# Performance work log

Hardware: AMD Instinct MI355X
Metric: run time of the kernel (lower is better)

Reference implementation:

```python
import jax, jax.numpy as jnp
import numpy as np

V, E, H = 32000, 256, 512
B, S, T = 32, 80, 80


def setup_inputs() -> dict:
    key = jax.random.key(0)
    ks = jax.random.split(key, 16)
    s = 0.05
    emb = jax.random.normal(ks[0], (V, E), jnp.float32) * s
    emb = emb.at[0].set(0.0)  # padding_idx=0 row is zero
    inp = {
        "src": jax.random.randint(ks[1], (B, S), 0, V),
        "tgt": jax.random.randint(ks[2], (B, T), 0, V),
        "emb": emb,
        "enc_Wih": jax.random.normal(ks[3], (3 * H, E), jnp.float32) * s,
        "enc_Whh": jax.random.normal(ks[4], (3 * H, H), jnp.float32) * s,
        "enc_bih": jax.random.normal(ks[5], (3 * H,), jnp.float32) * s,
        "enc_bhh": jax.random.normal(ks[6], (3 * H,), jnp.float32) * s,
        "dec_Wih": jax.random.normal(ks[7], (3 * H, E), jnp.float32) * s,
        "dec_Whh": jax.random.normal(ks[8], (3 * H, H), jnp.float32) * s,
        "dec_bih": jax.random.normal(ks[9], (3 * H,), jnp.float32) * s,
        "dec_bhh": jax.random.normal(ks[10], (3 * H,), jnp.float32) * s,
        "out_W": jax.random.normal(ks[11], (V, 2 * H), jnp.float32) * s,
        "out_b": jax.random.normal(ks[12], (V,), jnp.float32) * s,
    }
    return inp


def _gru_cell(x, h, Wih, Whh, bih, bhh):
    # PyTorch GRU cell: gates ordered (r, z, n)
    gi = x @ Wih.T + bih          # (B, 3H)
    gh = h @ Whh.T + bhh          # (B, 3H)
    i_r, i_z, i_n = jnp.split(gi, 3, axis=-1)
    h_r, h_z, h_n = jnp.split(gh, 3, axis=-1)
    r = jax.nn.sigmoid(i_r + h_r)
    z = jax.nn.sigmoid(i_z + h_z)
    n = jnp.tanh(i_n + r * h_n)
    return (1.0 - z) * n + z * h


def reference(src, tgt, emb, enc_Wih, enc_Whh, enc_bih, enc_bhh,
              dec_Wih, dec_Whh, dec_bih, dec_bhh, out_W, out_b):
    Bsz, Tlen = tgt.shape

    # ---- encoder: single-layer GRU over src ----
    x_src = emb[src]                              # (B, S, E)
    h0 = jnp.zeros((Bsz, H), x_src.dtype)

    def enc_step(h, x_t):
        h = _gru_cell(x_t, h, enc_Wih, enc_Whh, enc_bih, enc_bhh)
        return h, h

    h_enc, enc_outs = jax.lax.scan(enc_step, h0, jnp.swapaxes(x_src, 0, 1))
    enc_outs = jnp.swapaxes(enc_outs, 0, 1)       # (B, S, H)

    # ---- decoder: teacher forcing (ratio=1.0), steps t=1..T-1 ----
    x_dec = emb[tgt[:, :-1]]                      # (B, T-1, E)

    def dec_step(h, x_t):
        h = _gru_cell(x_t, h, dec_Wih, dec_Whh, dec_bih, dec_bhh)
        # Luong dot attention on new hidden state
        scores = jnp.einsum('bsh,bh->bs', enc_outs, h)
        aw = jax.nn.softmax(scores, axis=1)
        ctx = jnp.einsum('bs,bsh->bh', aw, enc_outs)
        combined = jnp.concatenate([h, ctx], axis=1)   # (B, 2H)
        step_logits = combined @ out_W.T + out_b       # (B, V)
        return h, step_logits

    _, step_logits = jax.lax.scan(dec_step, h_enc, jnp.swapaxes(x_dec, 0, 1))
    step_logits = jnp.swapaxes(step_logits, 0, 1)      # (B, T-1, V)

    # logits[:, 0, :] stays zero, matching the torch module
    logits = jnp.concatenate(
        [jnp.zeros((Bsz, 1, V), step_logits.dtype), step_logits], axis=1)
    return logits
```

## Files before the change

kernel.cpp:

```cpp
#include <hip/hip_runtime.h>

#define VV 32000
#define EE 256
#define HH 512
#define BB 32
#define SS 80
#define TT 80

typedef __attribute__((ext_vector_type(8))) _Float16 half8;
typedef __attribute__((ext_vector_type(4))) _Float16 half4;
typedef __attribute__((ext_vector_type(4))) float floatx4;
typedef unsigned long long u64;

__device__ __forceinline__ void gload16(const _Float16* g, _Float16* l) {
  __builtin_amdgcn_global_load_lds((const __attribute__((address_space(1))) void*)g,
                                   (__attribute__((address_space(3))) void*)l, 16, 0, 0);
}

__device__ __forceinline__ u64 aload(const u64* p) {
  return __hip_atomic_load(p, __ATOMIC_RELAXED, __HIP_MEMORY_SCOPE_AGENT);
}
__device__ __forceinline__ void astore(u64* p, u64 v) {
  __hip_atomic_store(p, v, __ATOMIC_RELAXED, __HIP_MEMORY_SCOPE_AGENT);
}

__device__ __forceinline__ unsigned pack15(unsigned short u) {
  return (u & 0x3FFFu) | ((u >> 1) & 0x4000u);
}
__device__ __forceinline__ unsigned short unpack15(unsigned v) {
  return (unsigned short)((v & 0x3FFFu) | ((v & 0x4000u) << 1));
}
__device__ __forceinline__ u64 unpack_word4(u64 a) {
  u64 o = 0;
#pragma unroll
  for (int i = 0; i < 4; ++i)
    o |= (u64)unpack15((unsigned)(a >> (15*i)) & 0x7FFFu) << (16*i);
  return o;
}

__device__ __forceinline__ float dot8(half8 a, half8 b, float c) {
  typedef __attribute__((ext_vector_type(2))) _Float16 half2v;
  half2v a0 = {a[0],a[1]}, a1 = {a[2],a[3]}, a2 = {a[4],a[5]}, a3 = {a[6],a[7]};
  half2v b0 = {b[0],b[1]}, b1 = {b[2],b[3]}, b2 = {b[4],b[5]}, b3 = {b[6],b[7]};
  c = __builtin_amdgcn_fdot2(a0, b0, c, false);
  c = __builtin_amdgcn_fdot2(a1, b1, c, false);
  c = __builtin_amdgcn_fdot2(a2, b2, c, false);
  c = __builtin_amdgcn_fdot2(a3, b3, c, false);
  return c;
}

__device__ __forceinline__ float sigm(float x) { return 1.f/(1.f + __expf(-x)); }
__device__ __forceinline__ float tanh_f(float x) { return 2.f/(1.f + __expf(-2.f*x)) - 1.f; }

__global__ __launch_bounds__(256) void gi_fused(
    const int* __restrict__ src, const int* __restrict__ tgt,
    const float* __restrict__ emb,
    const float* __restrict__ eWih, const float* __restrict__ ebih,
    const float* __restrict__ dWih, const float* __restrict__ dbih,
    float* __restrict__ giE, float* __restrict__ giD)
{
  __shared__ _Float16 As[4096];
  __shared__ _Float16 Bs[4096];
  const int tid = threadIdx.x;
  const int lane = tid & 63;
  const int wv = tid >> 6;
  const int wr = wv >> 1, wc = wv & 1;
  const int mt = blockIdx.y;
  const bool isE = blockIdx.x < 12;
  const int nt = isE ? blockIdx.x : blockIdx.x - 12;
  const float* Wih = isE ? eWih : dWih;
  const float* bih = isE ? ebih : dbih;
  float* gi = isE ? giE : giD;
  floatx4 acc[4][4];
#pragma unroll
  for (int i=0;i<4;++i)
#pragma unroll
    for (int j=0;j<4;++j) acc[i][j] = (floatx4){0.f,0.f,0.f,0.f};
  const int r2 = tid >> 1, cb = (tid & 1) * 16;
  const int R = mt*128 + r2;
  int tok = -1;
  if (isE) tok = src[R];
  else if (R < 2528) { const int b_ = R/79, tt = R - b_*79; tok = tgt[b_*80 + tt]; }
  const float* arow = (tok >= 0) ? emb + (size_t)tok*EE : nullptr;
  const float* brow = Wih + (size_t)(nt*128 + r2)*EE;
  const int g8 = (lane >> 4) * 8;
  const int lr = lane & 15;
  for (int kb = 0; kb < EE; kb += 32) {
    __syncthreads();
    if (arow) {
#pragma unroll
      for (int q = 0; q < 4; ++q) {
        const floatx4 va = *(const floatx4*)(arow + kb + cb + q*4);
#pragma unroll
        for (int e = 0; e < 4; ++e) As[r2*32 + cb + q*4 + e] = (_Float16)va[e];
      }
    } else {
#pragma unroll
      for (int q = 0; q < 16; ++q) As[r2*32 + cb + q] = (_Float16)0.f;
    }
#pragma unroll
    for (int q = 0; q < 4; ++q) {
      const floatx4 vb = *(const floatx4*)(brow + kb + cb + q*4);
#pragma unroll
      for (int e = 0; e < 4; ++e) Bs[r2*32 + cb + q*4 + e] = (_Float16)vb[e];
    }
    __syncthreads();
    half8 af[4], bf[4];
#pragma unroll
    for (int i=0;i<4;++i) af[i] = *(const half8*)(As + (wr*64 + i*16 + lr)*32 + g8);
#pragma unroll
    for (int j=0;j<4;++j) bf[j] = *(const half8*)(Bs + (wc*64 + j*16 + lr)*32 + g8);
#pragma unroll
    for (int i=0;i<4;++i)
#pragma unroll
      for (int j=0;j<4;++j)
        acc[i][j] = __builtin_amdgcn_mfma_f32_16x16x32_f16(af[i], bf[j], acc[i][j], 0,0,0);
  }
  const int rm = 4*(lane>>4);
#pragma unroll
  for (int i=0;i<4;++i)
#pragma unroll
    for (int r=0;r<4;++r) {
      const int row = mt*128 + wr*64 + i*16 + rm + r;
      if (isE || row < 2528) {
#pragma unroll
        for (int j=0;j<4;++j) {
          const int col = nt*128 + wc*64 + j*16 + lr;
          gi[(size_t)row*1536 + col] = acc[i][j][r] + bih[col];
        }
      }
    }
}

__global__ __launch_bounds__(256) void logits_gemm(
    const _Float16* __restrict__ A,
    const float* __restrict__ Bw,
    const float* __restrict__ bias, float* __restrict__ out)
{
  const int p = blockIdx.x;
  const int x = p & 7, s = p >> 3;
  const int nt = x + 8*(s / 20);
  const int mt = s % 20;
  if (nt >= 250) return;
  __shared__ _Float16 As[4096];
  __shared__ _Float16 Bs[4096];
  const int tid = threadIdx.x;
  const int lane = tid & 63;
  const int wv = tid >> 6;
  const int wr = wv >> 1, wc = wv & 1;
  floatx4 acc[4][4];
#pragma unroll
  for (int i=0;i<4;++i)
#pragma unroll
    for (int j=0;j<4;++j) acc[i][j] = (floatx4){0.f,0.f,0.f,0.f};
  const int srow = lane >> 2;
  const int scol = (lane & 3) * 8;
  const _Float16* Ab = A + (size_t)(mt*128)*1024;
  const int r2 = tid >> 1, cb = (tid & 1) * 16;
  const float* brow = Bw + (size_t)(nt*128 + r2)*1024;
  const int g8 = (lane >> 4) * 8;
  const int lr = lane & 15;
  for (int kb = 0; kb < 1024; kb += 32) {
    __syncthreads();
#pragma unroll
    for (int cc = 0; cc < 2; ++cc) {
      const int c = wv*2 + cc;
      gload16(Ab + (size_t)(c*16 + srow)*1024 + kb + scol, As + c*512);
    }
#pragma unroll
    for (int q = 0; q < 4; ++q) {
      const floatx4 vb = *(const floatx4*)(brow + kb + cb + q*4);
#pragma unroll
      for (int e = 0; e < 4; ++e) Bs[r2*32 + cb + q*4 + e] = (_Float16)vb[e];
    }
    __syncthreads();
    half8 af[4], bf[4];
#pragma unroll
    for (int i=0;i<4;++i) af[i] = *(const half8*)(As + (wr*64 + i*16 + lr)*32 + g8);
#pragma unroll
    for (int j=0;j<4;++j) bf[j] = *(const half8*)(Bs + (wc*64 + j*16 + lr)*32 + g8);
#pragma unroll
    for (int i=0;i<4;++i)
#pragma unroll
      for (int j=0;j<4;++j)
        acc[i][j] = __builtin_amdgcn_mfma_f32_16x16x32_f16(af[i], bf[j], acc[i][j], 0,0,0);
  }
  const int rm = 4*(lane>>4);
#pragma unroll
  for (int i=0;i<4;++i)
#pragma unroll
    for (int r=0;r<4;++r) {
      const int row = mt*128 + wr*64 + i*16 + rm + r;
#pragma unroll
      for (int j=0;j<4;++j) {
        const int col = nt*128 + wc*64 + j*16 + lr;
        if (row < 2528) {
          const int b = row / 79;
          const int t = row - b*79;
          out[(size_t)(b*80 + t + 1)*VV + col] = acc[i][j][r] + bias[col];
        } else {
          out[(size_t)((row - 2528)*80)*VV + col] = 0.f;
        }
      }
    }
}

#define SEQ_SMEM (80*512*2 + 512*2 + 512*2 + 3*64*8*4 + 2*80*4)
__global__ __launch_bounds__(512) void seq_pb(
    const float* __restrict__ eWhh, const float* __restrict__ dWhh,
    const float* __restrict__ ebhh, const float* __restrict__ dbhh,
    const float* __restrict__ giE, const float* __restrict__ giD,
    u64* __restrict__ hx,
    _Float16* __restrict__ comb)
{
  extern __shared__ char smem[];
  _Float16* eo_l = (_Float16*)smem;
  _Float16* hbuf = eo_l + 80*512;
  _Float16* hatt = hbuf + 512;
  float* part = (float*)(hatt + 512);
  float* sc = part + 3*64*8;
  float* aw = sc + 80;

  const int bi = blockIdx.x;
  const int q = bi >> 5, b = bi & 31;
  const int tid = threadIdx.x;
  const int lane = tid & 63;
  const int wv = tid >> 6;
  const int jl = tid & 63;
  const int kq = tid >> 6;
  const int j  = q*64 + jl;

  half8 wreg[3][8];
  auto loadW = [&](const float* W){
#pragma unroll
    for (int g = 0; g < 3; ++g)
#pragma unroll
      for (int c = 0; c < 8; ++c) {
        const float* s8 = W + ((size_t)(g*512 + j))*512 + kq*64 + c*8;
        const floatx4 a = *(const floatx4*)s8;
        const floatx4 d = *(const floatx4*)(s8 + 4);
        half8 h;
        h[0]=(_Float16)a[0]; h[1]=(_Float16)a[1]; h[2]=(_Float16)a[2]; h[3]=(_Float16)a[3];
        h[4]=(_Float16)d[0]; h[5]=(_Float16)d[1]; h[6]=(_Float16)d[2]; h[7]=(_Float16)d[3];
        wreg[g][c] = h;
      }
  };

  auto consume = [&](int slotR, u64 rtag){
    if (tid < 112) {
      const int m = tid + (tid >= q*16 ? 16 : 0);
      const u64* sp = hx + (size_t)slotR*4096 + b*128 + m;
      u64 v = aload(sp);
      int guard = 0;
      while ((v >> 60) != rtag && guard < (1<<22)) { v = aload(sp); ++guard; }
      *(u64*)&hbuf[m*4] = unpack_word4(v);
    }
    __syncthreads();
  };
  auto publish = [&](int slotW, u64 wtag){
    if (tid < 16) {
      const int m = q*16 + tid;
      u64 wq = wtag << 60;
#pragma unroll
      for (int e = 0; e < 4; ++e) {
        union { _Float16 h; unsigned short u; } cv; cv.h = hbuf[m*4 + e];
        wq |= (u64)pack15(cv.u) << (15*e);
      }
      astore(hx + (size_t)slotW*4096 + b*128 + m, wq);
    }
  };

  float hp = 0.f;
  auto gru = [&](float gr_, float gz_, float gn_, float bR, float bZ, float bN){
    half8 hv[8];
#pragma unroll
    for (int c = 0; c < 8; ++c) hv[c] = *(const half8*)&hbuf[kq*64 + c*8];
    float p0 = 0.f, p1 = 0.f, p2 = 0.f;
#pragma unroll
    for (int c = 0; c < 8; ++c) {
      p0 = dot8(wreg[0][c], hv[c], p0);
      p1 = dot8(wreg[1][c], hv[c], p1);
      p2 = dot8(wreg[2][c], hv[c], p2);
    }
    part[(0*64 + jl)*8 + kq] = p0;
    part[(1*64 + jl)*8 + kq] = p1;
    part[(2*64 + jl)*8 + kq] = p2;
    __syncthreads();
    if (tid < 64) {
      float a0 = 0.f, a1 = 0.f, a2 = 0.f;
#pragma unroll
      for (int e = 0; e < 8; ++e) {
        a0 += part[(0*64 + tid)*8 + e];
        a1 += part[(1*64 + tid)*8 + e];
        a2 += part[(2*64 + tid)*8 + e];
      }
      const float rg = sigm(gr_ + a0 + bR);
      const float zg = sigm(gz_ + a1 + bZ);
      const float ng = tanh_f(gn_ + rg*(a2 + bN));
      const float hn = (1.f - zg)*ng + zg*hp;
      hp = hn;
      hbuf[q*64 + tid] = (_Float16)hn;
    }
    __syncthreads();
  };

  auto attention = [&](int trow){
    const half8 hf = *(const half8*)&hatt[lane*8];
#pragma unroll 2
    for (int i = 0; i < 10; ++i) {
      const int s = wv*10 + i;
      const half8 ev = *(const half8*)&eo_l[s*512 + lane*8];
      float pt = dot8(ev, hf, 0.f);
#pragma unroll
      for (int o = 32; o; o >>= 1) pt += __shfl_xor(pt, o);
      if (lane == 0) sc[s] = pt;
    }
    __syncthreads();
    if (wv == 0) {
      const float v0 = sc[lane];
      const float v1 = (lane < 16) ? sc[64+lane] : -1e30f;
      float m = fmaxf(v0, v1);
#pragma unroll
      for (int o = 32; o; o >>= 1) m = fmaxf(m, __shfl_xor(m, o));
      const float e0 = __expf(v0 - m);
      const float e1 = (lane < 16) ? __expf(v1 - m) : 0.f;
      float ssum = e0 + e1;
#pragma unroll
      for (int o = 32; o; o >>= 1) ssum += __shfl_xor(ssum, o);
      const float inv = 1.f/ssum;
      aw[lane] = e0*inv;
      if (lane < 16) aw[64+lane] = e1*inv;
    }
    __syncthreads();
    if (tid < 64) {
      float c = 0.f;
#pragma unroll 8
      for (int s = 0; s < SS; ++s) c += aw[s] * (float)eo_l[s*512 + q*64 + tid];
      _Float16* cr = comb + ((size_t)b*79 + trow)*1024;
      cr[q*64 + tid]       = hatt[q*64 + tid];
      cr[512 + q*64 + tid] = (_Float16)c;
    }
    __syncthreads();
  };

  if (tid < 128) *(u64*)&hbuf[tid*4] = 0ull;
  loadW(eWhh);
  float ebR=0.f, ebZ=0.f, ebN=0.f, dbR=0.f, dbZ=0.f, dbN=0.f;
  if (tid < 64) {
    ebR = ebhh[j]; ebZ = ebhh[512+j]; ebN = ebhh[1024+j];
    dbR = dbhh[j]; dbZ = dbhh[512+j]; dbN = dbhh[1024+j];
  }
  __syncthreads();

  for (int k = 0; k < SS; ++k) {
    float gr_=0.f, gz_=0.f, gn_=0.f;
    if (tid < 64) {
      const float* gi = giE + ((size_t)b*SS + k)*1536;
      gr_ = gi[j]; gz_ = gi[512+j]; gn_ = gi[1024+j];
    }
    consume(k & 1, (u64)(k & 15));
    if (k > 0 && tid < 128)
      *(u64*)&eo_l[(k-1)*512 + tid*4] = *(const u64*)&hbuf[tid*4];
    gru(gr_, gz_, gn_, ebR, ebZ, ebN);
    publish((k+1) & 1, (u64)((k+1) & 15));
  }

  loadW(dWhh);

  for (int t = 0; t < TT-1; ++t) {
    const int k = 80 + t;
    float gr_=0.f, gz_=0.f, gn_=0.f;
    if (tid < 64) {
      const float* gi = giD + ((size_t)b*79 + t)*1536;
      gr_ = gi[j]; gz_ = gi[512+j]; gn_ = gi[1024+j];
    }
    consume(k & 1, (u64)(k & 15));
    if (tid < 128) {
      if (t == 0) *(u64*)&eo_l[79*512 + tid*4] = *(const u64*)&hbuf[tid*4];
      else        *(u64*)&hatt[tid*4]          = *(const u64*)&hbuf[tid*4];
    }
    gru(gr_, gz_, gn_, dbR, dbZ, dbN);
    publish((k+1) & 1, (u64)((k+1) & 15));
    if (t > 0) attention(t-1);
  }

  if (tid < 112) {
    const int m = tid + (tid >= q*16 ? 16 : 0);
    const u64* sp = hx + (size_t)4096 + b*128 + m;
    u64 v = aload(sp);
    int guard = 0;
    while ((v >> 60) != 15ull && guard < (1<<22)) { v = aload(sp); ++guard; }
    *(u64*)&hbuf[m*4] = unpack_word4(v);
  }
  __syncthreads();
  if (tid < 128) *(u64*)&hatt[tid*4] = *(const u64*)&hbuf[tid*4];
  __syncthreads();
  attention(TT-2);
}

extern "C" void kernel_launch(void* const* d_in, const int* in_sizes, int n_in,
                              void* d_out, int out_size, void* d_ws, size_t ws_size,
                              hipStream_t stream) {
  (void)in_sizes; (void)n_in; (void)out_size; (void)ws_size;
  const int*   src  = (const int*)d_in[0];
  const int*   tgt  = (const int*)d_in[1];
  const float* emb  = (const float*)d_in[2];
  const float* eWih = (const float*)d_in[3];
  const float* eWhh = (const float*)d_in[4];
  const float* ebih = (const float*)d_in[5];
  const float* ebhh = (const float*)d_in[6];
  const float* dWih = (const float*)d_in[7];
  const float* dWhh = (const float*)d_in[8];
  const float* dbih = (const float*)d_in[9];
  const float* dbhh = (const float*)d_in[10];
  const float* outW = (const float*)d_in[11];
  const float* outb = (const float*)d_in[12];
  float* out = (float*)d_out;

  char* p = (char*)d_ws;
  auto alloc = [&](size_t n){ char* r = p; p += (n + 255) & ~(size_t)255; return r; };
  float*    giE  = (float*)alloc((size_t)2560*1536*4);
  float*    giD  = (float*)alloc((size_t)2560*1536*4);
  u64*      hx   = (u64*)alloc((size_t)2*32*128*8);
  _Float16* comb = (_Float16*)alloc((size_t)2560*1024*2);

  hipMemsetAsync(hx, 0, (size_t)2*32*128*8, stream);
  gi_fused<<<dim3(24,20), 256, 0, stream>>>(src, tgt, emb, eWih, ebih,
                                            dWih, dbih, giE, giD);
  hipFuncSetAttribute((const void*)seq_pb,
                      hipFuncAttributeMaxDynamicSharedMemorySize, SEQ_SMEM);
  seq_pb<<<256, 512, SEQ_SMEM, stream>>>(eWhh, dWhh, ebhh, dbhh, giE, giD,
                                         hx, comb);
  logits_gemm<<<5120, 256, 0, stream>>>(comb, outW, outb, out);
}
```

Baseline: 1.083 ms.

## Pre-convert output weights to fp16 in prep kernel and load via LDS DMA

Adds 512 extra blocks to the input-gate GEMM launch (renamed prep_all) that convert out_W from fp32 to fp16 into a workspace buffer. The logits GEMM then streams B tiles with global_load_lds directly instead of loading fp32 and converting into LDS in every tile. This removes the repeated fp32 read and conversion across the 20 M-tiles that reuse each weight tile. The cost is an extra full pass writing 64MB fp16 in the prep stage.

```diff
diff --git a/kernel.cpp b/kernel.cpp
--- a/kernel.cpp
+++ b/kernel.cpp
@@ -52,22 +52,41 @@
 __device__ __forceinline__ float sigm(float x) { return 1.f/(1.f + __expf(-x)); }
 __device__ __forceinline__ float tanh_f(float x) { return 2.f/(1.f + __expf(-2.f*x)) - 1.f; }
 
-__global__ __launch_bounds__(256) void gi_fused(
+__global__ __launch_bounds__(256) void prep_all(
     const int* __restrict__ src, const int* __restrict__ tgt,
     const float* __restrict__ emb,
     const float* __restrict__ eWih, const float* __restrict__ ebih,
     const float* __restrict__ dWih, const float* __restrict__ dbih,
+    const float* __restrict__ outW, _Float16* __restrict__ oWh,
     float* __restrict__ giE, float* __restrict__ giD)
 {
+  const int pblk = blockIdx.x;
+  const int tid = threadIdx.x;
+
+  if (pblk >= 480) {
+    const int pid = pblk - 480;
+    const long total8 = (long)VV*1024/8;
+    for (long i = (long)pid*256 + tid; i < total8; i += 512L*256) {
+      const float* s_ = outW + i*8;
+      const floatx4 a = *(const floatx4*)s_;
+      const floatx4 b = *(const floatx4*)(s_ + 4);
+      half8 h;
+      h[0]=(_Float16)a[0]; h[1]=(_Float16)a[1]; h[2]=(_Float16)a[2]; h[3]=(_Float16)a[3];
+      h[4]=(_Float16)b[0]; h[5]=(_Float16)b[1]; h[6]=(_Float16)b[2]; h[7]=(_Float16)b[3];
+      *(half8*)(oWh + i*8) = h;
+    }
+    return;
+  }
+
   __shared__ _Float16 As[4096];
   __shared__ _Float16 Bs[4096];
-  const int tid = threadIdx.x;
   const int lane = tid & 63;
   const int wv = tid >> 6;
   const int wr = wv >> 1, wc = wv & 1;
-  const int mt = blockIdx.y;
-  const bool isE = blockIdx.x < 12;
-  const int nt = isE ? blockIdx.x : blockIdx.x - 12;
+  const int mt = pblk / 24;
+  const int ntx = pblk % 24;
+  const bool isE = ntx < 12;
+  const int nt = isE ? ntx : ntx - 12;
   const float* Wih = isE ? eWih : dWih;
   const float* bih = isE ? ebih : dbih;
   float* gi = isE ? giE : giD;
@@ -133,8 +152,7 @@
 }
 
 __global__ __launch_bounds__(256) void logits_gemm(
-    const _Float16* __restrict__ A,
-    const float* __restrict__ Bw,
+    const _Float16* __restrict__ A, const _Float16* __restrict__ Bm,
     const float* __restrict__ bias, float* __restrict__ out)
 {
   const int p = blockIdx.x;
@@ -156,8 +174,7 @@
   const int srow = lane >> 2;
   const int scol = (lane & 3) * 8;
   const _Float16* Ab = A + (size_t)(mt*128)*1024;
-  const int r2 = tid >> 1, cb = (tid & 1) * 16;
-  const float* brow = Bw + (size_t)(nt*128 + r2)*1024;
+  const _Float16* Bb = Bm + (size_t)(nt*128)*1024;
   const int g8 = (lane >> 4) * 8;
   const int lr = lane & 15;
   for (int kb = 0; kb < 1024; kb += 32) {
@@ -166,12 +183,7 @@
     for (int cc = 0; cc < 2; ++cc) {
       const int c = wv*2 + cc;
       gload16(Ab + (size_t)(c*16 + srow)*1024 + kb + scol, As + c*512);
-    }
-#pragma unroll
-    for (int q = 0; q < 4; ++q) {
-      const floatx4 vb = *(const floatx4*)(brow + kb + cb + q*4);
-#pragma unroll
-      for (int e = 0; e < 4; ++e) Bs[r2*32 + cb + q*4 + e] = (_Float16)vb[e];
+      gload16(Bb + (size_t)(c*16 + srow)*1024 + kb + scol, Bs + c*512);
     }
     __syncthreads();
     half8 af[4], bf[4];
@@ -419,17 +431,18 @@
 
   char* p = (char*)d_ws;
   auto alloc = [&](size_t n){ char* r = p; p += (n + 255) & ~(size_t)255; return r; };
+  _Float16* oWh  = (_Float16*)alloc((size_t)VV*1024*2);
   float*    giE  = (float*)alloc((size_t)2560*1536*4);
   float*    giD  = (float*)alloc((size_t)2560*1536*4);
   u64*      hx   = (u64*)alloc((size_t)2*32*128*8);
   _Float16* comb = (_Float16*)alloc((size_t)2560*1024*2);
 
   hipMemsetAsync(hx, 0, (size_t)2*32*128*8, stream);
-  gi_fused<<<dim3(24,20), 256, 0, stream>>>(src, tgt, emb, eWih, ebih,
-                                            dWih, dbih, giE, giD);
+  prep_all<<<992, 256, 0, stream>>>(src, tgt, emb, eWih, ebih, dWih, dbih,
+                                    outW, oWh, giE, giD);
   hipFuncSetAttribute((const void*)seq_pb,
                       hipFuncAttributeMaxDynamicSharedMemorySize, SEQ_SMEM);
   seq_pb<<<256, 512, SEQ_SMEM, stream>>>(eWhh, dWhh, ebhh, dbhh, giE, giD,
                                          hx, comb);
-  logits_gemm<<<5120, 256, 0, stream>>>(comb, outW, outb, out);
-}
+  logits_gemm<<<5120, 256, 0, stream>>>(comb, oWh, outb, out);
+}
```

Result: faster. 967.6 us, median of 2 (-10.7%).
